# Kernel optimization log

Measured on AMD Instinct MI355X. Metric: run time of the kernel, lower is better.

The kernel has to match this reference:

```python
import jax, jax.numpy as jnp
import numpy as np

G = 512  # canvas resolution (init arg)

def setup_inputs() -> dict:
    key = jax.random.key(0)
    k1, k2 = jax.random.split(key)
    strokes = jax.random.uniform(k1, (32, 8, 2), dtype=jnp.float32)   # [S,P,2] in [0,1]
    thicknesses = jax.random.uniform(k2, (32,), dtype=jnp.float32)    # [S]
    return {"strokes": strokes, "thicknesses": thicknesses}

def reference(strokes, thicknesses):
    # strokes: [S,P,2], thicknesses: [S]. Vectorized version of the per-stroke loop.
    g = jnp.float32(G)
    s = jnp.clip(strokes, 0.0, 1.0) * g                      # [S,P,2] pixel coords
    t = jnp.maximum(thicknesses * 2.0 + 0.5, 0.5)            # [S] stroke thickness
    v = s[:, :-1][:, :, None, None, :]                       # [S,P-1,1,1,2] segment starts
    w = s[:, 1:][:, :, None, None, :]                        # [S,P-1,1,1,2] segment ends
    idx = jnp.arange(G, dtype=jnp.float32)
    xs, ys = jnp.meshgrid(idx, idx, indexing='ij')
    p = jnp.stack((xs, ys), axis=-1)[None, None]             # [1,1,G,G,2] grid coords
    e = w - v                                                # segment direction
    d2 = jnp.sum(e * e, axis=-1)                             # [S,P-1,1,1] squared length
    pv = p - v                                               # [S,P-1,G,G,2]
    frac = jnp.clip(jnp.sum(pv * e, axis=-1) / (d2 + 1e-5), 0.0, 1.0)  # [S,P-1,G,G]
    dist = jnp.linalg.norm(pv - frac[..., None] * e, axis=-1)  # point-to-segment distance
    darkness = jnp.min(dist, axis=1) / (2.0 * t[:, None, None])  # [S,G,G] min over segments
    return jnp.minimum(jnp.min(darkness, axis=0), 1.0)          # min over strokes vs ones-grid
```

## Files before the change

kernel.cpp:

```cpp
#include <hip/hip_runtime.h>


#define NSEG 224
#define TILE_I 16
#define TILE_J 32

__global__ __launch_bounds__(256) void render_kernel(
    const float* __restrict__ strokes,
    const float* __restrict__ thick,
    float* __restrict__ out)
{
    __shared__ float4 sseg[NSEG];
    __shared__ float2 smul[NSEG];
    __shared__ int cnt;
    const int tid = threadIdx.x;

    const int tile_j = blockIdx.x & 15;
    const int tile_i = blockIdx.x >> 4;
    const int i0 = tile_i * TILE_I;
    const int j0 = tile_j * TILE_J;
    const float ccx = (float)i0 + 7.5f;
    const float ccy = (float)j0 + 15.5f;

    if (tid == 0) cnt = 0;
    __syncthreads();

    if (tid < NSEG) {
        const int s = tid / 7;
        const int k = tid - s * 7;
        const int base = (s * 8 + k) * 2;
        float ax = strokes[base + 0];
        float ay = strokes[base + 1];
        float bx = strokes[base + 2];
        float by = strokes[base + 3];
        ax = fminf(fmaxf(ax, 0.0f), 1.0f) * 512.0f;
        ay = fminf(fmaxf(ay, 0.0f), 1.0f) * 512.0f;
        bx = fminf(fmaxf(bx, 0.0f), 1.0f) * 512.0f;
        by = fminf(fmaxf(by, 0.0f), 1.0f) * 512.0f;
        const float ex = bx - ax;
        const float ey = by - ay;
        const float d2 = ex * ex + ey * ey;
        const float inv = 1.0f / (d2 + 1e-5f);
        const float t  = fmaxf(thick[s] * 2.0f + 0.5f, 0.5f);
        const float pvx = ccx - ax;
        const float pvy = ccy - ay;
        float f = fmaf(pvy, ey, pvx * ex) * inv;
        f = fminf(fmaxf(f, 0.0f), 1.0f);
        const float dx = fmaf(-f, ex, pvx);
        const float dy = fmaf(-f, ey, pvy);
        const float d2c = fmaf(dy, dy, dx * dx);
        const float thr = 2.0f * t + 18.0f;
        if (d2c < thr * thr) {
            const int idx = atomicAdd(&cnt, 1);
            sseg[idx] = make_float4(ax, ay, ex, ey);
            smul[idx] = make_float2(inv, 1.0f / (4.0f * t * t));
        }
    }
    __syncthreads();
    const int n_kept = cnt;

    const int pi = i0 + (tid >> 4);
    const int pj = j0 + ((tid & 15) << 1);
    const float px  = (float)pi;
    const float py0 = (float)pj;
    const float py1 = py0 + 1.0f;

    float acc0 = 4.0f, acc1 = 4.0f;
    for (int g = 0; g < n_kept; ++g) {
        const float4 sg = sseg[g];
        const float2 ms = smul[g];
        const float pvx  = px  - sg.x;
        const float pvy0 = py0 - sg.y;
        const float pvy1 = py1 - sg.y;
        const float pe   = pvx * sg.z;
        float f0 = fmaf(pvy0, sg.w, pe) * ms.x;
        float f1 = fmaf(pvy1, sg.w, pe) * ms.x;
        f0 = fminf(fmaxf(f0, 0.0f), 1.0f);
        f1 = fminf(fmaxf(f1, 0.0f), 1.0f);
        const float dx0 = fmaf(-f0, sg.z, pvx);
        const float dy0 = fmaf(-f0, sg.w, pvy0);
        const float dx1 = fmaf(-f1, sg.z, pvx);
        const float dy1 = fmaf(-f1, sg.w, pvy1);
        const float q0 = fmaf(dy0, dy0, dx0 * dx0);
        const float q1 = fmaf(dy1, dy1, dx1 * dx1);
        acc0 = fminf(acc0, q0 * ms.y);
        acc1 = fminf(acc1, q1 * ms.y);
    }

    const float o0 = fminf(sqrtf(acc0), 1.0f);
    const float o1 = fminf(sqrtf(acc1), 1.0f);
    *reinterpret_cast<float2*>(out + (pi << 9) + pj) = make_float2(o0, o1);
}

extern "C" void kernel_launch(void* const* d_in, const int* in_sizes, int n_in,
                              void* d_out, int out_size, void* d_ws, size_t ws_size,
                              hipStream_t stream) {
    const float* strokes = (const float*)d_in[0];
    const float* thick   = (const float*)d_in[1];
    float* out = (float*)d_out;
    hipLaunchKernelGGL(render_kernel, dim3(512), dim3(256), 0, stream,
                       strokes, thick, out);
}
```

Before: 55.93 us.

## Use smaller 16x16 tiles with tighter culling and premultiplied segment direction

Shrinks each block's tile from 16x32 to 16x16 with one pixel per thread and doubles the grid to 1024 blocks. The culling radius around the tile centre is tightened to match, so each block keeps fewer segments. Segment direction is premultiplied by the inverse squared length, which removes one multiply per pixel-segment pair. The cost is that each thread no longer shares work across two pixels, there are more blocks each paying the setup phase, and the shared-memory reads are wider.

```diff
diff --git a/kernel.cpp b/kernel.cpp
--- a/kernel.cpp
+++ b/kernel.cpp
@@ -2,25 +2,23 @@
 
 
 #define NSEG 224
-#define TILE_I 16
-#define TILE_J 32
 
 __global__ __launch_bounds__(256) void render_kernel(
     const float* __restrict__ strokes,
     const float* __restrict__ thick,
     float* __restrict__ out)
 {
-    __shared__ float4 sseg[NSEG];
-    __shared__ float2 smul[NSEG];
+    __shared__ float4 sa[NSEG];
+    __shared__ float4 sb[NSEG];
     __shared__ int cnt;
     const int tid = threadIdx.x;
 
-    const int tile_j = blockIdx.x & 15;
-    const int tile_i = blockIdx.x >> 4;
-    const int i0 = tile_i * TILE_I;
-    const int j0 = tile_j * TILE_J;
+    const int tile_j = blockIdx.x & 31;
+    const int tile_i = blockIdx.x >> 5;
+    const int i0 = tile_i << 4;
+    const int j0 = tile_j << 4;
     const float ccx = (float)i0 + 7.5f;
-    const float ccy = (float)j0 + 15.5f;
+    const float ccy = (float)j0 + 7.5f;
 
     if (tid == 0) cnt = 0;
     __syncthreads();
@@ -49,47 +47,36 @@
         const float dx = fmaf(-f, ex, pvx);
         const float dy = fmaf(-f, ey, pvy);
         const float d2c = fmaf(dy, dy, dx * dx);
-        const float thr = 2.0f * t + 18.0f;
+        const float thr = 2.0f * t + 11.0f;
         if (d2c < thr * thr) {
             const int idx = atomicAdd(&cnt, 1);
-            sseg[idx] = make_float4(ax, ay, ex, ey);
-            smul[idx] = make_float2(inv, 1.0f / (4.0f * t * t));
+            sa[idx] = make_float4(ax, ay, ex, ey);
+            sb[idx] = make_float4(ex * inv, ey * inv, 1.0f / (4.0f * t * t), 0.0f);
         }
     }
     __syncthreads();
     const int n_kept = cnt;
 
     const int pi = i0 + (tid >> 4);
-    const int pj = j0 + ((tid & 15) << 1);
-    const float px  = (float)pi;
-    const float py0 = (float)pj;
-    const float py1 = py0 + 1.0f;
+    const int pj = j0 + (tid & 15);
+    const float px = (float)pi;
+    const float py = (float)pj;
 
-    float acc0 = 4.0f, acc1 = 4.0f;
+    float acc = 4.0f;
     for (int g = 0; g < n_kept; ++g) {
-        const float4 sg = sseg[g];
-        const float2 ms = smul[g];
-        const float pvx  = px  - sg.x;
-        const float pvy0 = py0 - sg.y;
-        const float pvy1 = py1 - sg.y;
-        const float pe   = pvx * sg.z;
-        float f0 = fmaf(pvy0, sg.w, pe) * ms.x;
-        float f1 = fmaf(pvy1, sg.w, pe) * ms.x;
-        f0 = fminf(fmaxf(f0, 0.0f), 1.0f);
-        f1 = fminf(fmaxf(f1, 0.0f), 1.0f);
-        const float dx0 = fmaf(-f0, sg.z, pvx);
-        const float dy0 = fmaf(-f0, sg.w, pvy0);
-        const float dx1 = fmaf(-f1, sg.z, pvx);
-        const float dy1 = fmaf(-f1, sg.w, pvy1);
-        const float q0 = fmaf(dy0, dy0, dx0 * dx0);
-        const float q1 = fmaf(dy1, dy1, dx1 * dx1);
-        acc0 = fminf(acc0, q0 * ms.y);
-        acc1 = fminf(acc1, q1 * ms.y);
+        const float4 A = sa[g];
+        const float4 B = sb[g];
+        const float pvx = px - A.x;
+        const float pvy = py - A.y;
+        float f = fmaf(pvy, B.y, pvx * B.x);
+        f = fminf(fmaxf(f, 0.0f), 1.0f);
+        const float dx = fmaf(-f, A.z, pvx);
+        const float dy = fmaf(-f, A.w, pvy);
+        const float q = fmaf(dy, dy, dx * dx);
+        acc = fminf(acc, q * B.z);
     }
 
-    const float o0 = fminf(sqrtf(acc0), 1.0f);
-    const float o1 = fminf(sqrtf(acc1), 1.0f);
-    *reinterpret_cast<float2*>(out + (pi << 9) + pj) = make_float2(o0, o1);
+    out[(pi << 9) + pj] = fminf(sqrtf(acc), 1.0f);
 }
 
 extern "C" void kernel_launch(void* const* d_in, const int* in_sizes, int n_in,
@@ -98,6 +85,6 @@
     const float* strokes = (const float*)d_in[0];
     const float* thick   = (const float*)d_in[1];
     float* out = (float*)d_out;
-    hipLaunchKernelGGL(render_kernel, dim3(512), dim3(256), 0, stream,
+    hipLaunchKernelGGL(render_kernel, dim3(1024), dim3(256), 0, stream,
                        strokes, thick, out);
 }
```

Measured after the change: 56.54 us. Within noise of the previous version (+1.1%).
